# Kernel tuning notes

Measured on AMD Instinct MI355X. Metric: run time of the kernel, lower is better.

The kernel has to match this reference:

```python
import jax, jax.numpy as jnp
import numpy as np

N_NODES = 8192
N_EDGES = 524288
IN_DIM = 256
HID1 = 128
HID2 = 64


def setup_inputs() -> dict:
    key = jax.random.key(0)
    ks = jax.random.split(key, 10)
    s = 0.05
    x = jax.random.normal(ks[0], (N_NODES, IN_DIM), dtype=jnp.float32)
    edge_index = jax.random.randint(ks[1], (2, N_EDGES), 0, N_NODES, dtype=jnp.int64)
    W1 = jax.random.normal(ks[2], (IN_DIM, HID1), dtype=jnp.float32) * s
    b1 = jnp.zeros((HID1,), dtype=jnp.float32)
    W2 = jax.random.normal(ks[3], (IN_DIM, HID1), dtype=jnp.float32) * s
    b2 = jnp.zeros((HID1,), dtype=jnp.float32)
    Wmu = jax.random.normal(ks[4], (2 * HID1, HID2), dtype=jnp.float32) * s
    bmu = jnp.zeros((HID2,), dtype=jnp.float32)
    Wlv = jax.random.normal(ks[5], (2 * HID1, HID2), dtype=jnp.float32) * s
    blv = jnp.zeros((HID2,), dtype=jnp.float32)
    return {"x": x, "edge_index": edge_index, "W1": W1, "b1": b1,
            "W2": W2, "b2": b2, "Wmu": Wmu, "bmu": bmu, "Wlv": Wlv, "blv": blv}


def _gcn(x, W, b, row, col, norm, n):
    # linear transform, edge-indexed gather, degree-normalized scale, scatter-add
    h = x @ W                                   # [N, out]
    msg = h[col] * norm[:, None]                # [E+N, out]
    agg = jax.ops.segment_sum(msg, row, num_segments=n)
    return agg + b


def reference(x, edge_index, W1, b1, W2, b2, Wmu, bmu, Wlv, blv):
    n = x.shape[0]
    loop = jnp.arange(n, dtype=edge_index.dtype)
    row = jnp.concatenate([edge_index[0], loop])   # add self-loops (GCNConv default)
    col = jnp.concatenate([edge_index[1], loop])
    deg = jax.ops.segment_sum(jnp.ones_like(row, dtype=x.dtype), row, num_segments=n)
    dinv = jnp.where(deg > 0, jax.lax.rsqrt(deg), 0.0)
    norm = dinv[row] * dinv[col]                   # symmetric D^-1/2 A_hat D^-1/2

    h1 = _gcn(x, W1, b1, row, col, norm, n)
    h2 = _gcn(x, W2, b2, row, col, norm, n)
    hc = jnp.concatenate([h1, h2], axis=1)         # [N, 2*HID1]
    mu = _gcn(hc, Wmu, bmu, row, col, norm, n)
    logvar = _gcn(hc, Wlv, blv, row, col, norm, n)
    z = mu                                         # eval-mode reparametrize -> mu
    adj = jax.nn.sigmoid(z @ z.T)                  # InnerProductDecoder.forward_all
    return adj, mu, logvar
```

## Files before the change

kernel.cpp:

```cpp
#include <hip/hip_runtime.h>
#include <hip/hip_bf16.h>

#define N_NODES 8192
#define N_EDGES 524288
#define TOT_EDGES (N_EDGES + N_NODES)
#define IN_DIM 256
#define HID1 128
#define HID2 64
#define DC 128
#define CAP 192

typedef __attribute__((ext_vector_type(8))) short bf16x8;
typedef __attribute__((ext_vector_type(4))) float f32x4;
typedef __attribute__((ext_vector_type(4))) int   i32x4;
typedef __attribute__((ext_vector_type(4))) unsigned short u16x4;

__device__ __forceinline__ float b2f(unsigned short u){
    unsigned int v = ((unsigned int)u) << 16;
    float f; __builtin_memcpy(&f, &v, 4); return f;
}
__device__ __forceinline__ unsigned short f2b(float f){
    __hip_bfloat16 h = __float2bfloat16(f);
    return *(unsigned short*)&h;
}


__global__ __launch_bounds__(256) void k_pre(const float* __restrict__ x, unsigned short* __restrict__ xbf,
                                             const float* __restrict__ W1, const float* __restrict__ W2,
                                             const float* __restrict__ Wmu, const float* __restrict__ Wlv,
                                             const float* __restrict__ b1, const float* __restrict__ b2,
                                             unsigned short* __restrict__ WcT, float* __restrict__ cvec,
                                             float* __restrict__ zbase){
    int b = blockIdx.x, t = threadIdx.x;
    if (b < 2048){
        int g = (b*256 + t)*4;
        f32x4 v = *(const f32x4*)(x + g);
        u16x4 o;
        #pragma unroll
        for (int j=0;j<4;j++) o[j] = f2b(v[j]);
        *(u16x4*)(xbf + g) = o;
    } else if (b < 2176){
        int r = (b - 2048)*2 + (t >> 7);
        int j = t & 127;
        const float* Wsel = (j < 64) ? Wmu : Wlv;
        int jj = j & 63;
        float acc = 0.f;
        for (int k=0;k<HID1;k++){
            acc += W1[r*HID1+k] * Wsel[k*HID2+jj] + W2[r*HID1+k] * Wsel[(HID1+k)*HID2+jj];
        }
        WcT[(size_t)j*IN_DIM + r] = f2b(acc);
        if (r == 0){
            float c = 0.f;
            for (int k=0;k<HID1;k++){
                c += b1[k]*Wsel[k*HID2+jj] + b2[k]*Wsel[(HID1+k)*HID2+jj];
            }
            cvec[j] = c;
        }
    } else {
        ((f32x4*)zbase)[(b-2176)*256 + t] = (f32x4){0.f,0.f,0.f,0.f};
    }
}


__global__ __launch_bounds__(256) void k_fill(const int* __restrict__ ei, int* __restrict__ fillc,
                                              unsigned short* __restrict__ slots){
    int e4 = (blockIdx.x*256 + threadIdx.x)*4;
    if (e4 >= TOT_EDGES) return;
    if (e4 < N_EDGES){
        i32x4 rr = *(const i32x4*)(ei + e4);
        i32x4 cc = *(const i32x4*)(ei + N_EDGES + e4);
        #pragma unroll
        for (int j=0;j<4;j++){
            int s = atomicAdd(&fillc[rr[j]], 1);
            if (s < CAP) slots[(size_t)rr[j]*CAP + s] = (unsigned short)cc[j];
        }
    } else {
        #pragma unroll
        for (int j=0;j<4;j++){
            int r = e4 - N_EDGES + j;
            int s = atomicAdd(&fillc[r], 1);
            if (s < CAP) slots[(size_t)r*CAP + s] = (unsigned short)r;
        }
    }
}


__global__ __launch_bounds__(256) void k_dinv_gemm(const int* __restrict__ fillc, float* __restrict__ dinv,
                                                   const unsigned short* __restrict__ xbf,
                                                   const unsigned short* __restrict__ WcT,
                                                   unsigned short* __restrict__ Ubf){
    int t = threadIdx.x;
    if (blockIdx.x == 0){
        int base = t*32;
        const i32x4* dp = (const i32x4*)(fillc + base);
        #pragma unroll
        for (int k=0;k<8;k++){
            i32x4 q = dp[k];
            f32x4 dv;
            #pragma unroll
            for (int j=0;j<4;j++) dv[j] = (q[j] > 0) ? rsqrtf((float)q[j]) : 0.f;
            *(f32x4*)(dinv + base + k*4) = dv;
        }
    } else {
        int l  = t & 63;
        int w  = t >> 6;
        int Ibase = (blockIdx.x - 1)*32;
        int Jbase = w*32;
        int lr = l & 15;
        int kg = l >> 4;
        f32x4 acc[2][2];
        #pragma unroll
        for (int mt=0;mt<2;mt++)
            #pragma unroll
            for (int nt=0;nt<2;nt++) acc[mt][nt] = (f32x4){0.f,0.f,0.f,0.f};
        #pragma unroll
        for (int kc=0; kc<IN_DIM/32; kc++){
            bf16x8 a[2], bb[2];
            #pragma unroll
            for (int mt=0;mt<2;mt++)
                a[mt] = *(const bf16x8*)(xbf + (size_t)(Ibase+mt*16+lr)*IN_DIM + kc*32 + kg*8);
            #pragma unroll
            for (int nt=0;nt<2;nt++)
                bb[nt] = *(const bf16x8*)(WcT + (size_t)(Jbase+nt*16+lr)*IN_DIM + kc*32 + kg*8);
            #pragma unroll
            for (int mt=0;mt<2;mt++)
                #pragma unroll
                for (int nt=0;nt<2;nt++)
                    acc[mt][nt] = __builtin_amdgcn_mfma_f32_16x16x32_bf16(a[mt], bb[nt], acc[mt][nt], 0, 0, 0);
        }
        #pragma unroll
        for (int mt=0;mt<2;mt++)
            #pragma unroll
            for (int r=0;r<4;r++){
                int grow = Ibase + mt*16 + kg*4 + r;
                #pragma unroll
                for (int nt=0;nt<2;nt++)
                    Ubf[(size_t)grow*DC + Jbase + nt*16 + lr] = f2b(acc[mt][nt][r]);
            }
    }
}


__global__ __launch_bounds__(256) void k_spmm(const unsigned short* __restrict__ IN,
                                              const unsigned short* __restrict__ slots,
                                              const int* __restrict__ fillc,
                                              const float* __restrict__ dinv,
                                              unsigned short* __restrict__ OUT){
    int tid = threadIdx.x;
    int i = blockIdx.x*4 + (tid >> 6);
    int l  = tid & 15;
    int eg = (tid >> 4) & 3;
    int deg = min(fillc[i], CAP);
    const unsigned short* sl = slots + (size_t)i*CAP;
    float acc[8] = {0.f,0.f,0.f,0.f,0.f,0.f,0.f,0.f};
    for (int e = eg; e < deg; e += 4){
        int c = sl[e];
        float wgt = dinv[c];
        bf16x8 v = *(const bf16x8*)(IN + (size_t)c*DC + l*8);
        #pragma unroll
        for (int j=0;j<8;j++) acc[j] += wgt * b2f((unsigned short)v[j]);
    }
    #pragma unroll
    for (int j=0;j<8;j++){
        acc[j] += __shfl_xor(acc[j], 16);
        acc[j] += __shfl_xor(acc[j], 32);
    }
    if (eg == 0){
        float di = dinv[i];
        bf16x8 o;
        #pragma unroll
        for (int j=0;j<8;j++) o[j] = (short)f2b(di*acc[j]);
        *(bf16x8*)(OUT + (size_t)i*DC + l*8) = o;
    }
}


__global__ __launch_bounds__(256) void k_spmm_out(const unsigned short* __restrict__ T,
                                                  const unsigned short* __restrict__ slots,
                                                  const int* __restrict__ fillc,
                                                  const float* __restrict__ dinv,
                                                  const float* __restrict__ cvec,
                                                  const float* __restrict__ bmu, const float* __restrict__ blv,
                                                  float* __restrict__ outMu, float* __restrict__ outLv,
                                                  unsigned short* __restrict__ muBf){
    int tid = threadIdx.x;
    int i = blockIdx.x*4 + (tid >> 6);
    int l  = tid & 15;
    int eg = (tid >> 4) & 3;
    int deg = min(fillc[i], CAP);
    const unsigned short* sl = slots + (size_t)i*CAP;
    float acc[8] = {0.f,0.f,0.f,0.f,0.f,0.f,0.f,0.f};
    float wsum = 0.f;
    for (int e = eg; e < deg; e += 4){
        int c = sl[e];
        float wgt = dinv[c];
        wsum += wgt;
        bf16x8 v = *(const bf16x8*)(T + (size_t)c*DC + l*8);
        #pragma unroll
        for (int j=0;j<8;j++) acc[j] += wgt * b2f((unsigned short)v[j]);
    }
    #pragma unroll
    for (int j=0;j<8;j++){
        acc[j] += __shfl_xor(acc[j], 16);
        acc[j] += __shfl_xor(acc[j], 32);
    }
    wsum += __shfl_xor(wsum, 16);
    wsum += __shfl_xor(wsum, 32);
    if (eg == 0){
        float di = dinv[i];
        float sv = di * wsum;
        float val[8];
        #pragma unroll
        for (int j=0;j<8;j++) val[j] = di*acc[j] + sv*cvec[l*8+j];
        if (l < 8){
            f32x4 v0, v1; bf16x8 o;
            #pragma unroll
            for (int j=0;j<8;j++){
                float vv = val[j] + bmu[l*8+j];
                if (j<4) v0[j] = vv; else v1[j-4] = vv;
                o[j] = (short)f2b(vv);
            }
            *(f32x4*)(outMu + (size_t)i*HID2 + l*8)     = v0;
            *(f32x4*)(outMu + (size_t)i*HID2 + l*8 + 4) = v1;
            *(bf16x8*)(muBf + (size_t)i*HID2 + l*8)     = o;
        } else {
            int d = (l-8)*8;
            f32x4 v0, v1;
            #pragma unroll
            for (int j=0;j<8;j++){
                float vv = val[j] + blv[d+j];
                if (j<4) v0[j] = vv; else v1[j-4] = vv;
            }
            *(f32x4*)(outLv + (size_t)i*HID2 + d)     = v0;
            *(f32x4*)(outLv + (size_t)i*HID2 + d + 4) = v1;
        }
    }
}


__global__ __launch_bounds__(256) void k_adj(const unsigned short* __restrict__ mu, float* __restrict__ adj){
    int t  = threadIdx.x;
    int l  = t & 63;
    int w  = t >> 6;
    int wr = w >> 1, wc = w & 1;
    int Ibase = blockIdx.y*128 + wr*64;
    int Jbase0 = blockIdx.x*128;
    int Jbase = Jbase0 + wc*64;
    int lr = l & 15;
    int kg = l >> 4;

    bf16x8 afr[4][2], bfr[4][2];
    #pragma unroll
    for (int mt=0; mt<4; mt++){
        const unsigned short* p = mu + (size_t)(Ibase + mt*16 + lr)*HID2 + kg*8;
        afr[mt][0] = *(const bf16x8*)(p);
        afr[mt][1] = *(const bf16x8*)(p + 32);
    }
    #pragma unroll
    for (int nt=0; nt<4; nt++){
        const unsigned short* p = mu + (size_t)(Jbase + nt*16 + lr)*HID2 + kg*8;
        bfr[nt][0] = *(const bf16x8*)(p);
        bfr[nt][1] = *(const bf16x8*)(p + 32);
    }

    f32x4 acc[4][4];
    #pragma unroll
    for (int mt=0; mt<4; mt++)
        #pragma unroll
        for (int nt=0; nt<4; nt++)
            acc[mt][nt] = (f32x4){0.f,0.f,0.f,0.f};

    #pragma unroll
    for (int kc=0; kc<2; kc++)
        #pragma unroll
        for (int mt=0; mt<4; mt++)
            #pragma unroll
            for (int nt=0; nt<4; nt++)
                acc[mt][nt] = __builtin_amdgcn_mfma_f32_16x16x32_bf16(afr[mt][kc], bfr[nt][kc], acc[mt][nt], 0, 0, 0);

    __shared__ float tile[64][132];
    int rowBlockBase = blockIdx.y*128;
    #pragma unroll
    for (int p=0; p<2; p++){
        if (wr == p){
            #pragma unroll
            for (int mt=0; mt<4; mt++)
                #pragma unroll
                for (int r=0; r<4; r++){
                    int row_local = mt*16 + kg*4 + r;
                    #pragma unroll
                    for (int nt=0; nt<4; nt++){
                        float v = acc[mt][nt][r];
                        tile[row_local][wc*64 + nt*16 + lr] = 1.f/(1.f + __expf(-v));
                    }
                }
        }
        __syncthreads();
        #pragma unroll
        for (int rep=0; rep<8; rep++){
            int row_r = rep*8 + (t >> 5);
            int col   = (t & 31)*4;
            f32x4 v = *(const f32x4*)&tile[row_r][col];
            int grow = rowBlockBase + p*64 + row_r;
            *(f32x4*)(adj + (size_t)grow*N_NODES + Jbase0 + col) = v;
        }
        __syncthreads();
    }
}


extern "C" void kernel_launch(void* const* d_in, const int* in_sizes, int n_in,
                              void* d_out, int out_size, void* d_ws, size_t ws_size,
                              hipStream_t stream){
    const float* x   = (const float*)d_in[0];
    const int*   ei  = (const int*)  d_in[1];
    const float* W1  = (const float*)d_in[2];
    const float* b1  = (const float*)d_in[3];
    const float* W2  = (const float*)d_in[4];
    const float* b2  = (const float*)d_in[5];
    const float* Wmu = (const float*)d_in[6];
    const float* bmu = (const float*)d_in[7];
    const float* Wlv = (const float*)d_in[8];
    const float* blv = (const float*)d_in[9];

    char* ws = (char*)d_ws;
    int*   fillc  = (int*)  (ws + 0);
    float* dinv   = (float*)(ws + 32768);
    unsigned short* WcT = (unsigned short*)(ws + 65536);
    float* cvec   = (float*)(ws + 131072);
    unsigned short* muBf = (unsigned short*)(ws + 131584);
    unsigned short* xbf  = (unsigned short*)(ws + 1180160);

    float* adj   = (float*)d_out;
    float* outMu = adj + (size_t)N_NODES*N_NODES;
    float* outLv = outMu + (size_t)N_NODES*HID2;

    unsigned short* Ubf   = (unsigned short*)adj;
    unsigned short* Tbf   = (unsigned short*)((char*)adj + 16*1024*1024);
    unsigned short* slots = (unsigned short*)((char*)adj + 32*1024*1024);

    k_pre      <<<2184, 256, 0, stream>>>(x, xbf, W1, W2, Wmu, Wlv, b1, b2, WcT, cvec, (float*)ws);
    k_fill     <<< 520, 256, 0, stream>>>(ei, fillc, slots);
    k_dinv_gemm<<< 257, 256, 0, stream>>>(fillc, dinv, xbf, WcT, Ubf);
    k_spmm     <<<N_NODES/4, 256, 0, stream>>>(Ubf, slots, fillc, dinv, Tbf);
    k_spmm_out <<<N_NODES/4, 256, 0, stream>>>(Tbf, slots, fillc, dinv, cvec, bmu, blv,
                                               outMu, outLv, muBf);
    k_adj      <<<dim3(N_NODES/128, N_NODES/128), 256, 0, stream>>>(muBf, adj);
}
```

Measured before the change: 154.6 us.

## Fuse edge fill with GEMM kernel, compute dinv inline, move sigmoid to store loop

Merges the edge-bucketing kernel and the x·Wc GEMM into one launch, since the two are independent. The separate dinv array and its kernel are dropped, and the SpMM kernels compute rsqrt of the degree count on the fly. The adjacency kernel now applies the sigmoid with a hardware reciprocal in the vectorised store loop instead of during the LDS write. This removes one launch and one dependent pass, at the cost of extra rsqrt work per gathered edge.

```diff
diff --git a/kernel.cpp b/kernel.cpp
--- a/kernel.cpp
+++ b/kernel.cpp
@@ -9,6 +9,7 @@
 #define HID2 64
 #define DC 128
 #define CAP 192
+#define FILL_BLK 520
 
 typedef __attribute__((ext_vector_type(8))) short bf16x8;
 typedef __attribute__((ext_vector_type(4))) float f32x4;
@@ -62,49 +63,35 @@
 }
 
 
-__global__ __launch_bounds__(256) void k_fill(const int* __restrict__ ei, int* __restrict__ fillc,
-                                              unsigned short* __restrict__ slots){
-    int e4 = (blockIdx.x*256 + threadIdx.x)*4;
-    if (e4 >= TOT_EDGES) return;
-    if (e4 < N_EDGES){
-        i32x4 rr = *(const i32x4*)(ei + e4);
-        i32x4 cc = *(const i32x4*)(ei + N_EDGES + e4);
-        #pragma unroll
-        for (int j=0;j<4;j++){
-            int s = atomicAdd(&fillc[rr[j]], 1);
-            if (s < CAP) slots[(size_t)rr[j]*CAP + s] = (unsigned short)cc[j];
-        }
-    } else {
-        #pragma unroll
-        for (int j=0;j<4;j++){
-            int r = e4 - N_EDGES + j;
-            int s = atomicAdd(&fillc[r], 1);
-            if (s < CAP) slots[(size_t)r*CAP + s] = (unsigned short)r;
-        }
-    }
-}
-
-
-__global__ __launch_bounds__(256) void k_dinv_gemm(const int* __restrict__ fillc, float* __restrict__ dinv,
+__global__ __launch_bounds__(256) void k_fill_gemm(const int* __restrict__ ei, int* __restrict__ fillc,
+                                                   unsigned short* __restrict__ slots,
                                                    const unsigned short* __restrict__ xbf,
                                                    const unsigned short* __restrict__ WcT,
                                                    unsigned short* __restrict__ Ubf){
-    int t = threadIdx.x;
-    if (blockIdx.x == 0){
-        int base = t*32;
-        const i32x4* dp = (const i32x4*)(fillc + base);
-        #pragma unroll
-        for (int k=0;k<8;k++){
-            i32x4 q = dp[k];
-            f32x4 dv;
-            #pragma unroll
-            for (int j=0;j<4;j++) dv[j] = (q[j] > 0) ? rsqrtf((float)q[j]) : 0.f;
-            *(f32x4*)(dinv + base + k*4) = dv;
+    int b = blockIdx.x, t = threadIdx.x;
+    if (b < FILL_BLK){
+        int e4 = (b*256 + t)*4;
+        if (e4 >= TOT_EDGES) return;
+        if (e4 < N_EDGES){
+            i32x4 rr = *(const i32x4*)(ei + e4);
+            i32x4 cc = *(const i32x4*)(ei + N_EDGES + e4);
+            #pragma unroll
+            for (int j=0;j<4;j++){
+                int s = atomicAdd(&fillc[rr[j]], 1);
+                if (s < CAP) slots[(size_t)rr[j]*CAP + s] = (unsigned short)cc[j];
+            }
+        } else {
+            #pragma unroll
+            for (int j=0;j<4;j++){
+                int r = e4 - N_EDGES + j;
+                int s = atomicAdd(&fillc[r], 1);
+                if (s < CAP) slots[(size_t)r*CAP + s] = (unsigned short)r;
+            }
         }
     } else {
         int l  = t & 63;
         int w  = t >> 6;
-        int Ibase = (blockIdx.x - 1)*32;
+        int Ibase = (b - FILL_BLK)*32;
         int Jbase = w*32;
         int lr = l & 15;
         int kg = l >> 4;
@@ -144,7 +131,6 @@
 __global__ __launch_bounds__(256) void k_spmm(const unsigned short* __restrict__ IN,
                                               const unsigned short* __restrict__ slots,
                                               const int* __restrict__ fillc,
-                                              const float* __restrict__ dinv,
                                               unsigned short* __restrict__ OUT){
     int tid = threadIdx.x;
     int i = blockIdx.x*4 + (tid >> 6);
@@ -155,7 +141,7 @@
     float acc[8] = {0.f,0.f,0.f,0.f,0.f,0.f,0.f,0.f};
     for (int e = eg; e < deg; e += 4){
         int c = sl[e];
-        float wgt = dinv[c];
+        float wgt = rsqrtf((float)fillc[c]);
         bf16x8 v = *(const bf16x8*)(IN + (size_t)c*DC + l*8);
         #pragma unroll
         for (int j=0;j<8;j++) acc[j] += wgt * b2f((unsigned short)v[j]);
@@ -166,7 +152,7 @@
         acc[j] += __shfl_xor(acc[j], 32);
     }
     if (eg == 0){
-        float di = dinv[i];
+        float di = rsqrtf((float)fillc[i]);
         bf16x8 o;
         #pragma unroll
         for (int j=0;j<8;j++) o[j] = (short)f2b(di*acc[j]);
@@ -178,7 +164,6 @@
 __global__ __launch_bounds__(256) void k_spmm_out(const unsigned short* __restrict__ T,
                                                   const unsigned short* __restrict__ slots,
                                                   const int* __restrict__ fillc,
-                                                  const float* __restrict__ dinv,
                                                   const float* __restrict__ cvec,
                                                   const float* __restrict__ bmu, const float* __restrict__ blv,
                                                   float* __restrict__ outMu, float* __restrict__ outLv,
@@ -193,7 +178,7 @@
     float wsum = 0.f;
     for (int e = eg; e < deg; e += 4){
         int c = sl[e];
-        float wgt = dinv[c];
+        float wgt = rsqrtf((float)fillc[c]);
         wsum += wgt;
         bf16x8 v = *(const bf16x8*)(T + (size_t)c*DC + l*8);
         #pragma unroll
@@ -207,7 +192,7 @@
     wsum += __shfl_xor(wsum, 16);
     wsum += __shfl_xor(wsum, 32);
     if (eg == 0){
-        float di = dinv[i];
+        float di = rsqrtf((float)fillc[i]);
         float sv = di * wsum;
         float val[8];
         #pragma unroll
@@ -289,10 +274,8 @@
                 for (int r=0; r<4; r++){
                     int row_local = mt*16 + kg*4 + r;
                     #pragma unroll
-                    for (int nt=0; nt<4; nt++){
-                        float v = acc[mt][nt][r];
-                        tile[row_local][wc*64 + nt*16 + lr] = 1.f/(1.f + __expf(-v));
-                    }
+                    for (int nt=0; nt<4; nt++)
+                        tile[row_local][wc*64 + nt*16 + lr] = acc[mt][nt][r];
                 }
         }
         __syncthreads();
@@ -301,8 +284,12 @@
             int row_r = rep*8 + (t >> 5);
             int col   = (t & 31)*4;
             f32x4 v = *(const f32x4*)&tile[row_r][col];
+            f32x4 o;
+            #pragma unroll
+            for (int j=0;j<4;j++)
+                o[j] = __builtin_amdgcn_rcpf(1.f + __expf(-v[j]));
             int grow = rowBlockBase + p*64 + row_r;
-            *(f32x4*)(adj + (size_t)grow*N_NODES + Jbase0 + col) = v;
+            *(f32x4*)(adj + (size_t)grow*N_NODES + Jbase0 + col) = o;
         }
         __syncthreads();
     }
@@ -325,11 +312,10 @@
 
     char* ws = (char*)d_ws;
     int*   fillc  = (int*)  (ws + 0);
-    float* dinv   = (float*)(ws + 32768);
-    unsigned short* WcT = (unsigned short*)(ws + 65536);
-    float* cvec   = (float*)(ws + 131072);
-    unsigned short* muBf = (unsigned short*)(ws + 131584);
-    unsigned short* xbf  = (unsigned short*)(ws + 1180160);
+    unsigned short* WcT = (unsigned short*)(ws + 32768);
+    float* cvec   = (float*)(ws + 98304);
+    unsigned short* muBf = (unsigned short*)(ws + 98816);
+    unsigned short* xbf  = (unsigned short*)(ws + 1147392);
 
     float* adj   = (float*)d_out;
     float* outMu = adj + (size_t)N_NODES*N_NODES;
@@ -340,10 +326,9 @@
     unsigned short* slots = (unsigned short*)((char*)adj + 32*1024*1024);
 
     k_pre      <<<2184, 256, 0, stream>>>(x, xbf, W1, W2, Wmu, Wlv, b1, b2, WcT, cvec, (float*)ws);
-    k_fill     <<< 520, 256, 0, stream>>>(ei, fillc, slots);
-    k_dinv_gemm<<< 257, 256, 0, stream>>>(fillc, dinv, xbf, WcT, Ubf);
-    k_spmm     <<<N_NODES/4, 256, 0, stream>>>(Ubf, slots, fillc, dinv, Tbf);
-    k_spmm_out <<<N_NODES/4, 256, 0, stream>>>(Tbf, slots, fillc, dinv, cvec, bmu, blv,
+    k_fill_gemm<<<FILL_BLK + 256, 256, 0, stream>>>(ei, fillc, slots, xbf, WcT, Ubf);
+    k_spmm     <<<N_NODES/4, 256, 0, stream>>>(Ubf, slots, fillc, Tbf);
+    k_spmm_out <<<N_NODES/4, 256, 0, stream>>>(Tbf, slots, fillc, cvec, bmu, blv,
                                                outMu, outLv, muBf);
     k_adj      <<<dim3(N_NODES/128, N_NODES/128), 256, 0, stream>>>(muBf, adj);
 }
```

Measured after the change: 133.0 us. 1.16x faster.
